# Performance work log

Hardware: AMD Instinct MI355X
Metric: run time of the kernel (lower is better)

Reference implementation:

```python
import jax, jax.numpy as jnp
import numpy as np

N = 100000   # nodes
E = 1600000  # edges (avg degree 16)
D = 256      # in_channels == out_channels
EPS = 1e-3   # Keras LayerNormalization default epsilon


def setup_inputs() -> dict:
    key = jax.random.key(0)
    k1, k2, k3 = jax.random.split(key, 3)
    x = jax.random.normal(k1, (N, D), dtype=jnp.float32)
    edge_index = jax.random.randint(k2, (2, E), 0, N, dtype=jnp.int32)
    W = jax.random.normal(k3, (D, D), dtype=jnp.float32) / np.float32(np.sqrt(D))
    b = jnp.zeros((D,), dtype=jnp.float32)
    gamma = jnp.ones((D,), dtype=jnp.float32)
    beta = jnp.zeros((D,), dtype=jnp.float32)
    return {"x": x, "edge_index": edge_index, "W": W, "b": b, "gamma": gamma, "beta": beta}


def reference(x, edge_index, W, b, gamma, beta):
    src, dst = edge_index[0], edge_index[1]
    n = x.shape[0]
    # in-degree with self-loop, symmetric GCN normalization 1/sqrt(d_i d_j)
    deg = jax.ops.segment_sum(jnp.ones((src.shape[0],), x.dtype), dst, num_segments=n) + 1.0
    norm = jax.lax.rsqrt(deg)               # [N]
    h = x @ W                               # [N, D] dense transform
    msg = h[src] * norm[src, None]          # gather + scale, [E, D]
    agg = jax.ops.segment_sum(msg, dst, num_segments=n) * norm[:, None]
    agg = agg + h * (norm * norm)[:, None] + b   # self-loop term + bias
    # residual (in_channels == out_channels) + layer norm
    y = x + agg
    mean = jnp.mean(y, axis=-1, keepdims=True)
    var = jnp.mean(jnp.square(y - mean), axis=-1, keepdims=True)
    return gamma * (y - mean) * jax.lax.rsqrt(var + EPS) + beta
```

## Files before the change

### kernel.cpp

```cpp
#include <hip/hip_runtime.h>


#define D_DIM 256
#define NPART 8
#define SLOTS 64

typedef __attribute__((ext_vector_type(8))) short short8;
typedef __attribute__((ext_vector_type(4))) float f32x4;
typedef __attribute__((ext_vector_type(2))) float f32x2;

__device__ __forceinline__ unsigned short f2bf(float f) {
    unsigned int u = __builtin_bit_cast(unsigned int, f);
    u = (u + 0x7fffu + ((u >> 16) & 1u)) >> 16;
    return (unsigned short)u;
}
__device__ __forceinline__ unsigned int pack2(float a, float b) {
    return (unsigned int)f2bf(a) | ((unsigned int)f2bf(b) << 16);
}

__device__ __forceinline__ unsigned int fp8e(float f) {
    float a = fminf(fmaxf(f, -448.f), 448.f);
    unsigned int u = __builtin_bit_cast(unsigned int, a);
    unsigned int s = (u >> 24) & 0x80u;
    int e = (int)((u >> 23) & 0xffu);
    unsigned int man = u & 0x7fffffu;
    if (e >= 121) {
        unsigned int mant = man >> 20;
        unsigned int rest = man & 0xfffffu;
        unsigned int inc = (rest > 0x80000u) || (rest == 0x80000u && (mant & 1u));
        unsigned int code = (((unsigned int)(e - 120)) << 3) | mant;
        code += inc;
        if (code > 0x7eu) code = 0x7eu;
        return s | code;
    }
    float m = fabsf(a) * 512.f;
    unsigned int mi = (unsigned int)rintf(m);
    return s | mi;
}

__global__ void prep(const float* __restrict__ W, unsigned short* __restrict__ Wt,
                     int* __restrict__ cnt, int N) {
    int i = blockIdx.x * blockDim.x + threadIdx.x;
    if (i < D_DIM * D_DIM) {
        int k = i >> 8, n = i & 255;
        Wt[(size_t)n * D_DIM + k] = f2bf(W[(size_t)k * D_DIM + n]);
    }
    if (i < N) cnt[i] = 0;
}

__global__ void fill_pad_part(const int* __restrict__ src, const int* __restrict__ dst,
                              int E, int* __restrict__ cnt, int* __restrict__ srcs_pad,
                              int npp) {
    const int part = blockIdx.x & (NPART - 1);
    const int bid  = blockIdx.x >> 3;
    const int nblk = gridDim.x >> 3;
    const int lo = part * npp, hi = lo + npp;
    for (int e = bid * blockDim.x + threadIdx.x; e < E; e += nblk * blockDim.x) {
        int d = dst[e];
        if (d >= lo && d < hi) {
            int pos = atomicAdd(&cnt[d], 1);
            if (pos < SLOTS) srcs_pad[(size_t)d * SLOTS + pos] = src[e];
        }
    }
}

__global__ void make_nrm(const int* __restrict__ cnt, float* __restrict__ nrm, int N) {
    int i = blockIdx.x * blockDim.x + threadIdx.x;
    if (i < N) nrm[i] = rsqrtf((float)cnt[i] + 1.0f);
}

#define GBM 128
#define GBK 32
#define LDK 40

__global__ __launch_bounds__(512) void gemm_mfma(
    const float* __restrict__ X, const unsigned short* __restrict__ Wt,
    const float* __restrict__ nrm, unsigned char* __restrict__ Hs8, int M) {
    __shared__ unsigned short As[2][GBM * LDK];
    __shared__ unsigned short Bs[2][D_DIM * LDK];

    const int t    = threadIdx.x;
    const int lane = t & 63;
    const int wave = t >> 6;
    const int wr   = wave >> 2, wc = wave & 3;
    const int m0   = blockIdx.x * GBM;

    const int arow = t >> 2;
    const int akc  = (t & 3) * 8;
    const int xr   = (m0 + arow < M) ? (m0 + arow) : (M - 1);
    const float* xp = X + (size_t)xr * D_DIM;
    const int bn0 = t >> 2,           bkc0 = (t & 3) * 8;
    const int bn1 = (t + 512) >> 2,   bkc1 = ((t + 512) & 3) * 8;

    {
        float4 a0 = *(const float4*)(xp + akc);
        float4 a1 = *(const float4*)(xp + akc + 4);
        uint4 A = {pack2(a0.x, a0.y), pack2(a0.z, a0.w),
                   pack2(a1.x, a1.y), pack2(a1.z, a1.w)};
        *(uint4*)&As[0][arow * LDK + akc] = A;
        *(uint4*)&Bs[0][bn0 * LDK + bkc0] = *(const uint4*)(Wt + (size_t)bn0 * D_DIM + bkc0);
        *(uint4*)&Bs[0][bn1 * LDK + bkc1] = *(const uint4*)(Wt + (size_t)bn1 * D_DIM + bkc1);
    }
    __syncthreads();

    f32x4 acc[4][4];
#pragma unroll
    for (int mi = 0; mi < 4; ++mi)
#pragma unroll
        for (int ni = 0; ni < 4; ++ni) acc[mi][ni] = (f32x4){0.f, 0.f, 0.f, 0.f};

    const int kp = (lane >> 4) * 8;

    for (int s = 0; s < 8; ++s) {
        float4 a0, a1;
        uint4  b0, b1;
        if (s < 7) {
            int kk = (s + 1) * GBK;
            a0 = *(const float4*)(xp + kk + akc);
            a1 = *(const float4*)(xp + kk + akc + 4);
            b0 = *(const uint4*)(Wt + (size_t)bn0 * D_DIM + kk + bkc0);
            b1 = *(const uint4*)(Wt + (size_t)bn1 * D_DIM + kk + bkc1);
        }

        short8 af[4], bfr[4];
#pragma unroll
        for (int mi = 0; mi < 4; ++mi)
            af[mi] = *(const short8*)&As[s & 1][(wr * 64 + mi * 16 + (lane & 15)) * LDK + kp];
#pragma unroll
        for (int ni = 0; ni < 4; ++ni)
            bfr[ni] = *(const short8*)&Bs[s & 1][(wc * 64 + ni * 16 + (lane & 15)) * LDK + kp];
#pragma unroll
        for (int mi = 0; mi < 4; ++mi)
#pragma unroll
            for (int ni = 0; ni < 4; ++ni)
                acc[mi][ni] = __builtin_amdgcn_mfma_f32_16x16x32_bf16(
                    af[mi], bfr[ni], acc[mi][ni], 0, 0, 0);

        if (s < 7) {
            uint4 A = {pack2(a0.x, a0.y), pack2(a0.z, a0.w),
                       pack2(a1.x, a1.y), pack2(a1.z, a1.w)};
            *(uint4*)&As[(s + 1) & 1][arow * LDK + akc] = A;
            *(uint4*)&Bs[(s + 1) & 1][bn0 * LDK + bkc0] = b0;
            *(uint4*)&Bs[(s + 1) & 1][bn1 * LDK + bkc1] = b1;
            __syncthreads();
        }
    }

#pragma unroll
    for (int mi = 0; mi < 4; ++mi) {
#pragma unroll
        for (int r = 0; r < 4; ++r) {
            int row = m0 + wr * 64 + mi * 16 + (lane >> 4) * 4 + r;
            if (row < M) {
                float nr = nrm[row];
#pragma unroll
                for (int ni = 0; ni < 4; ++ni) {
                    int col = wc * 64 + ni * 16 + (lane & 15);
                    Hs8[(size_t)row * D_DIM + col] =
                        (unsigned char)fp8e(acc[mi][ni][r] * nr);
                }
            }
        }
    }
}

__global__ __launch_bounds__(256) void agg_ln(
    const float* __restrict__ X, const unsigned char* __restrict__ Hs8,
    const int* __restrict__ cnt, const int* __restrict__ srcs_pad,
    const float* __restrict__ nrm, const float* __restrict__ bvec,
    const float* __restrict__ gamma, const float* __restrict__ beta,
    float* __restrict__ out, int N) {
    const int wave = (blockIdx.x * blockDim.x + threadIdx.x) >> 6;
    const int lane = threadIdx.x & 63;
    if (wave >= N) return;
    const int i = wave;

    auto ldrow = [&](int s) -> unsigned int {
        return *((const unsigned int*)(Hs8 + (size_t)s * D_DIM) + lane);
    };

    unsigned int hv = ldrow(i);
    f32x2 lo = __builtin_amdgcn_cvt_pk_f32_fp8(hv, false);
    f32x2 hi = __builtin_amdgcn_cvt_pk_f32_fp8(hv, true);
    float ax = lo.x, ay = lo.y, az = hi.x, aw = hi.y;

    auto accum = [&](unsigned int v) {
        f32x2 l = __builtin_amdgcn_cvt_pk_f32_fp8(v, false);
        f32x2 h = __builtin_amdgcn_cvt_pk_f32_fp8(v, true);
        ax += l.x; ay += l.y; az += h.x; aw += h.y;
    };

    const int* sp = srcs_pad + (size_t)i * SLOTS;
    const int ci = min(cnt[i], SLOTS);

    int e = 0;
    for (; e + 16 <= ci; e += 16) {
        int ss[16];
        unsigned int hh[16];
#pragma unroll
        for (int j = 0; j < 16; ++j) ss[j] = __builtin_amdgcn_readfirstlane(sp[e + j]);
#pragma unroll
        for (int j = 0; j < 16; ++j) hh[j] = ldrow(ss[j]);
#pragma unroll
        for (int j = 0; j < 16; ++j) accum(hh[j]);
    }
    for (; e + 8 <= ci; e += 8) {
        int ss[8];
        unsigned int hh[8];
#pragma unroll
        for (int j = 0; j < 8; ++j) ss[j] = __builtin_amdgcn_readfirstlane(sp[e + j]);
#pragma unroll
        for (int j = 0; j < 8; ++j) hh[j] = ldrow(ss[j]);
#pragma unroll
        for (int j = 0; j < 8; ++j) accum(hh[j]);
    }
    for (; e + 4 <= ci; e += 4) {
        int ss[4];
        unsigned int hh[4];
#pragma unroll
        for (int j = 0; j < 4; ++j) ss[j] = __builtin_amdgcn_readfirstlane(sp[e + j]);
#pragma unroll
        for (int j = 0; j < 4; ++j) hh[j] = ldrow(ss[j]);
#pragma unroll
        for (int j = 0; j < 4; ++j) accum(hh[j]);
    }
    for (; e < ci; ++e) accum(ldrow(__builtin_amdgcn_readfirstlane(sp[e])));

    const float ni = nrm[i];
    float4 xv = reinterpret_cast<const float4*>(X)[(size_t)i * 64 + lane];
    float4 bv = reinterpret_cast<const float4*>(bvec)[lane];

    float4 y;
    y.x = xv.x + ax * ni + bv.x;
    y.y = xv.y + ay * ni + bv.y;
    y.z = xv.z + az * ni + bv.z;
    y.w = xv.w + aw * ni + bv.w;

    float s1 = y.x + y.y + y.z + y.w;
    float s2 = y.x * y.x + y.y * y.y + y.z * y.z + y.w * y.w;
#pragma unroll
    for (int off = 32; off > 0; off >>= 1) {
        s1 += __shfl_xor(s1, off);
        s2 += __shfl_xor(s2, off);
    }
    const float mean = s1 * (1.0f / 256.0f);
    const float var  = s2 * (1.0f / 256.0f) - mean * mean;
    const float rstd = rsqrtf(var + 1e-3f);

    float4 gv = reinterpret_cast<const float4*>(gamma)[lane];
    float4 be = reinterpret_cast<const float4*>(beta)[lane];
    float4 o;
    o.x = gv.x * (y.x - mean) * rstd + be.x;
    o.y = gv.y * (y.y - mean) * rstd + be.y;
    o.z = gv.z * (y.z - mean) * rstd + be.z;
    o.w = gv.w * (y.w - mean) * rstd + be.w;
    reinterpret_cast<float4*>(out)[(size_t)i * 64 + lane] = o;
}

extern "C" void kernel_launch(void* const* d_in, const int* in_sizes, int n_in,
                              void* d_out, int out_size, void* d_ws, size_t ws_size,
                              hipStream_t stream) {
    const float* x     = (const float*)d_in[0];
    const int*   ei    = (const int*)d_in[1];
    const float* W     = (const float*)d_in[2];
    const float* bvec  = (const float*)d_in[3];
    const float* gamma = (const float*)d_in[4];
    const float* beta  = (const float*)d_in[5];
    float*       out   = (float*)d_out;

    const int D = in_sizes[3];
    const int N = in_sizes[0] / D;
    const int E = in_sizes[1] / 2;
    const int* src = ei;
    const int* dst = ei + E;

    char* w = (char*)d_ws;
    size_t off = 0;
    auto alloc = [&](size_t bytes) -> void* {
        void* p = w + off;
        off = (off + bytes + 255) & ~(size_t)255;
        return p;
    };
    unsigned char*  Hs8      = (unsigned char*)alloc((size_t)N * D);
    unsigned short* Wt       = (unsigned short*)alloc((size_t)D * D * sizeof(unsigned short));
    float*          nrm      = (float*)alloc((size_t)N * sizeof(float));
    int*            cnt      = (int*)alloc((size_t)N * sizeof(int));
    int*            srcs_pad = (int*)alloc((size_t)N * SLOTS * sizeof(int));
    (void)ws_size;

    const int npp = (N + NPART - 1) / NPART;

    prep<<<(N + 255) / 256, 256, 0, stream>>>(W, Wt, cnt, N);
    fill_pad_part<<<2048, 256, 0, stream>>>(src, dst, E, cnt, srcs_pad, npp);
    make_nrm<<<(N + 255) / 256, 256, 0, stream>>>(cnt, nrm, N);

    gemm_mfma<<<(N + GBM - 1) / GBM, 512, 0, stream>>>(x, Wt, nrm, Hs8, N);

    int nwblocks = (N + 3) / 4;
    agg_ln<<<nwblocks, 256, 0, stream>>>(x, Hs8, cnt, srcs_pad, nrm, bvec,
                                         gamma, beta, out, N);
}
```

Baseline: 211.9 us.

## Run edge bucketing concurrently with GEMM and apply source norms during aggregation

Merges the edge-fill kernel into the GEMM launch as extra blocks, so padded-CSR construction overlaps with the dense transform. The separate normalization kernel goes away: the GEMM stores unscaled fp8 rows, and the aggregation kernel computes rsqrt(cnt+1) per source and per destination on the fly, using FMA accumulation. This removes two launches and a dependency barrier. In exchange it adds a per-edge cnt gather in the aggregation loop, drops the 16-wide unroll, and changes fp8 quantization since rows are no longer pre-scaled.

```diff
diff --git a/kernel.cpp b/kernel.cpp
--- a/kernel.cpp
+++ b/kernel.cpp
@@ -4,6 +4,7 @@
 #define D_DIM 256
 #define NPART 8
 #define SLOTS 64
+#define NFILL 1024
 
 typedef __attribute__((ext_vector_type(8))) short short8;
 typedef __attribute__((ext_vector_type(4))) float f32x4;
@@ -48,38 +49,35 @@
     if (i < N) cnt[i] = 0;
 }
 
-__global__ void fill_pad_part(const int* __restrict__ src, const int* __restrict__ dst,
-                              int E, int* __restrict__ cnt, int* __restrict__ srcs_pad,
-                              int npp) {
-    const int part = blockIdx.x & (NPART - 1);
-    const int bid  = blockIdx.x >> 3;
-    const int nblk = gridDim.x >> 3;
-    const int lo = part * npp, hi = lo + npp;
-    for (int e = bid * blockDim.x + threadIdx.x; e < E; e += nblk * blockDim.x) {
-        int d = dst[e];
-        if (d >= lo && d < hi) {
-            int pos = atomicAdd(&cnt[d], 1);
-            if (pos < SLOTS) srcs_pad[(size_t)d * SLOTS + pos] = src[e];
-        }
-    }
-}
-
-__global__ void make_nrm(const int* __restrict__ cnt, float* __restrict__ nrm, int N) {
-    int i = blockIdx.x * blockDim.x + threadIdx.x;
-    if (i < N) nrm[i] = rsqrtf((float)cnt[i] + 1.0f);
-}
-
 #define GBM 128
 #define GBK 32
 #define LDK 40
 
-__global__ __launch_bounds__(512) void gemm_mfma(
+__global__ __launch_bounds__(512) void mega(
     const float* __restrict__ X, const unsigned short* __restrict__ Wt,
-    const float* __restrict__ nrm, unsigned char* __restrict__ Hs8, int M) {
+    unsigned char* __restrict__ Hs8,
+    const int* __restrict__ src, const int* __restrict__ dst, int E,
+    int* __restrict__ cnt, int* __restrict__ srcs_pad,
+    int npp, int M, int ntiles) {
     __shared__ unsigned short As[2][GBM * LDK];
     __shared__ unsigned short Bs[2][D_DIM * LDK];
 
-    const int t    = threadIdx.x;
+    const int t = threadIdx.x;
+
+    if (blockIdx.x >= ntiles) {
+        const int part = blockIdx.x & (NPART - 1);
+        const int lf   = (blockIdx.x - ntiles) >> 3;
+        const int lo = part * npp, hi = lo + npp;
+        for (int e = lf * 512 + t; e < E; e += (NFILL / 8) * 512) {
+            int d = dst[e];
+            if (d >= lo && d < hi) {
+                int pos = atomicAdd(&cnt[d], 1);
+                if (pos < SLOTS) srcs_pad[(size_t)d * SLOTS + pos] = src[e];
+            }
+        }
+        return;
+    }
+
     const int lane = t & 63;
     const int wave = t >> 6;
     const int wr   = wave >> 2, wc = wave & 3;
@@ -89,8 +87,8 @@
     const int akc  = (t & 3) * 8;
     const int xr   = (m0 + arow < M) ? (m0 + arow) : (M - 1);
     const float* xp = X + (size_t)xr * D_DIM;
-    const int bn0 = t >> 2,           bkc0 = (t & 3) * 8;
-    const int bn1 = (t + 512) >> 2,   bkc1 = ((t + 512) & 3) * 8;
+    const int bn0 = t >> 2,         bkc0 = (t & 3) * 8;
+    const int bn1 = (t + 512) >> 2, bkc1 = ((t + 512) & 3) * 8;
 
     {
         float4 a0 = *(const float4*)(xp + akc);
@@ -152,12 +150,10 @@
         for (int r = 0; r < 4; ++r) {
             int row = m0 + wr * 64 + mi * 16 + (lane >> 4) * 4 + r;
             if (row < M) {
-                float nr = nrm[row];
 #pragma unroll
                 for (int ni = 0; ni < 4; ++ni) {
                     int col = wc * 64 + ni * 16 + (lane & 15);
-                    Hs8[(size_t)row * D_DIM + col] =
-                        (unsigned char)fp8e(acc[mi][ni][r] * nr);
+                    Hs8[(size_t)row * D_DIM + col] = (unsigned char)fp8e(acc[mi][ni][r]);
                 }
             }
         }
@@ -167,9 +163,8 @@
 __global__ __launch_bounds__(256) void agg_ln(
     const float* __restrict__ X, const unsigned char* __restrict__ Hs8,
     const int* __restrict__ cnt, const int* __restrict__ srcs_pad,
-    const float* __restrict__ nrm, const float* __restrict__ bvec,
-    const float* __restrict__ gamma, const float* __restrict__ beta,
-    float* __restrict__ out, int N) {
+    const float* __restrict__ bvec, const float* __restrict__ gamma,
+    const float* __restrict__ beta, float* __restrict__ out, int N) {
     const int wave = (blockIdx.x * blockDim.x + threadIdx.x) >> 6;
     const int lane = threadIdx.x & 63;
     if (wave >= N) return;
@@ -178,55 +173,58 @@
     auto ldrow = [&](int s) -> unsigned int {
         return *((const unsigned int*)(Hs8 + (size_t)s * D_DIM) + lane);
     };
-
+    auto nrm_of = [&](int s) -> float {
+        return rsqrtf((float)cnt[s] + 1.0f);
+    };
+
+    const float ni = nrm_of(i);
     unsigned int hv = ldrow(i);
     f32x2 lo = __builtin_amdgcn_cvt_pk_f32_fp8(hv, false);
     f32x2 hi = __builtin_amdgcn_cvt_pk_f32_fp8(hv, true);
-    float ax = lo.x, ay = lo.y, az = hi.x, aw = hi.y;
-
-    auto accum = [&](unsigned int v) {
+    float ax = lo.x * ni, ay = lo.y * ni, az = hi.x * ni, aw = hi.y * ni;
+
+    auto accum = [&](unsigned int v, float w) {
         f32x2 l = __builtin_amdgcn_cvt_pk_f32_fp8(v, false);
         f32x2 h = __builtin_amdgcn_cvt_pk_f32_fp8(v, true);
-        ax += l.x; ay += l.y; az += h.x; aw += h.y;
+        ax = fmaf(l.x, w, ax); ay = fmaf(l.y, w, ay);
+        az = fmaf(h.x, w, az); aw = fmaf(h.y, w, aw);
     };
 
     const int* sp = srcs_pad + (size_t)i * SLOTS;
     const int ci = min(cnt[i], SLOTS);
 
     int e = 0;
-    for (; e + 16 <= ci; e += 16) {
-        int ss[16];
-        unsigned int hh[16];
-#pragma unroll
-        for (int j = 0; j < 16; ++j) ss[j] = __builtin_amdgcn_readfirstlane(sp[e + j]);
-#pragma unroll
-        for (int j = 0; j < 16; ++j) hh[j] = ldrow(ss[j]);
-#pragma unroll
-        for (int j = 0; j < 16; ++j) accum(hh[j]);
-    }
     for (; e + 8 <= ci; e += 8) {
         int ss[8];
         unsigned int hh[8];
+        float ww[8];
 #pragma unroll
         for (int j = 0; j < 8; ++j) ss[j] = __builtin_amdgcn_readfirstlane(sp[e + j]);
 #pragma unroll
         for (int j = 0; j < 8; ++j) hh[j] = ldrow(ss[j]);
 #pragma unroll
-        for (int j = 0; j < 8; ++j) accum(hh[j]);
+        for (int j = 0; j < 8; ++j) ww[j] = nrm_of(ss[j]);
+#pragma unroll
+        for (int j = 0; j < 8; ++j) accum(hh[j], ww[j]);
     }
     for (; e + 4 <= ci; e += 4) {
         int ss[4];
         unsigned int hh[4];
+        float ww[4];
 #pragma unroll
         for (int j = 0; j < 4; ++j) ss[j] = __builtin_amdgcn_readfirstlane(sp[e + j]);
 #pragma unroll
         for (int j = 0; j < 4; ++j) hh[j] = ldrow(ss[j]);
 #pragma unroll
-        for (int j = 0; j < 4; ++j) accum(hh[j]);
-    }
-    for (; e < ci; ++e) accum(ldrow(__builtin_amdgcn_readfirstlane(sp[e])));
-
-    const float ni = nrm[i];
+        for (int j = 0; j < 4; ++j) ww[j] = nrm_of(ss[j]);
+#pragma unroll
+        for (int j = 0; j < 4; ++j) accum(hh[j], ww[j]);
+    }
+    for (; e < ci; ++e) {
+        int s = __builtin_amdgcn_readfirstlane(sp[e]);
+        accum(ldrow(s), nrm_of(s));
+    }
+
     float4 xv = reinterpret_cast<const float4*>(X)[(size_t)i * 64 + lane];
     float4 bv = reinterpret_cast<const float4*>(bvec)[lane];
 
@@ -283,20 +281,18 @@
     };
     unsigned char*  Hs8      = (unsigned char*)alloc((size_t)N * D);
     unsigned short* Wt       = (unsigned short*)alloc((size_t)D * D * sizeof(unsigned short));
-    float*          nrm      = (float*)alloc((size_t)N * sizeof(float));
     int*            cnt      = (int*)alloc((size_t)N * sizeof(int));
     int*            srcs_pad = (int*)alloc((size_t)N * SLOTS * sizeof(int));
     (void)ws_size;
 
-    const int npp = (N + NPART - 1) / NPART;
+    const int npp    = (N + NPART - 1) / NPART;
+    const int ntiles = (N + GBM - 1) / GBM;
 
     prep<<<(N + 255) / 256, 256, 0, stream>>>(W, Wt, cnt, N);
-    fill_pad_part<<<2048, 256, 0, stream>>>(src, dst, E, cnt, srcs_pad, npp);
-    make_nrm<<<(N + 255) / 256, 256, 0, stream>>>(cnt, nrm, N);
-
-    gemm_mfma<<<(N + GBM - 1) / GBM, 512, 0, stream>>>(x, Wt, nrm, Hs8, N);
+    mega<<<ntiles + NFILL, 512, 0, stream>>>(x, Wt, Hs8, src, dst, E,
+                                             cnt, srcs_pad, npp, N, ntiles);
 
     int nwblocks = (N + 3) / 4;
-    agg_ln<<<nwblocks, 256, 0, stream>>>(x, Hs8, cnt, srcs_pad, nrm, bvec,
+    agg_ln<<<nwblocks, 256, 0, stream>>>(x, Hs8, cnt, srcs_pad, bvec,
                                          gamma, beta, out, N);
 }
```

Result: faster. 203.9 us (-3.8%).
